# Performance work log

Measured on AMD Instinct MI355X. Metric: run time of the kernel, lower is better.

Reference implementation:

```python
import jax, jax.numpy as jnp
import numpy as np
from jax import lax

KS = 11          # kernel_size
SIGMA = 1.5
MAX_VAL = 1.0
K1, K2 = 0.01, 0.03


def _gauss2d(ks=KS, sigma=SIGMA):
    x = np.arange(ks, dtype=np.float64) - ks // 2
    g = np.exp(-(x ** 2) / (2.0 * sigma ** 2))
    g = g / g.sum()
    return np.outer(g, g).astype(np.float32)  # [ks, ks]


def _bilinear_matrix(n_in, n_out):
    # align_corners=True bilinear resize as a linear map [n_out, n_in]
    pos = np.arange(n_out, dtype=np.float64) * (n_in - 1) / (n_out - 1)
    i0 = np.floor(pos).astype(np.int64)
    i1 = np.minimum(i0 + 1, n_in - 1)
    w = (pos - i0).astype(np.float32)
    M = np.zeros((n_out, n_in), dtype=np.float32)
    M[np.arange(n_out), i0] += 1.0 - w
    M[np.arange(n_out), i1] += w
    return jnp.asarray(M)


def setup_inputs() -> dict:
    key = jax.random.key(0)
    k1, k2 = jax.random.split(key)
    inp = jax.random.uniform(k1, (32, 3, 384, 384), dtype=jnp.float32)
    tgt = jax.random.uniform(k2, (32, 3, 512, 512), dtype=jnp.float32)
    return {"input": inp, "target": tgt}


def _ssim_loss(input, target):
    B, C, Hi, Wi = input.shape
    Ho, Wo = target.shape[-2], target.shape[-1]
    # bilinear align_corners interpolation of input to target spatial size
    A = _bilinear_matrix(Hi, Ho)  # [Ho, Hi]
    Bm = _bilinear_matrix(Wi, Wo)  # [Wo, Wi]
    img1 = jnp.einsum('oh,bchw,pw->bcop', A, input, Bm)
    img2 = target

    w2d = jnp.asarray(_gauss2d())
    window = jnp.broadcast_to(w2d, (C, 1, KS, KS))  # depthwise kernel [C,1,k,k]

    def dwconv(x):
        return lax.conv_general_dilated(
            x, window, window_strides=(1, 1), padding='VALID',
            feature_group_count=C,
            dimension_numbers=('NCHW', 'OIHW', 'NCHW'))

    mu1 = dwconv(img1)
    mu2 = dwconv(img2)
    mu1_sq = mu1 * mu1
    mu2_sq = mu2 * mu2
    mu1_mu2 = mu1 * mu2
    sigma1_sq = dwconv(img1 * img1) - mu1_sq
    sigma2_sq = dwconv(img2 * img2) - mu2_sq
    sigma12 = dwconv(img1 * img2) - mu1_mu2

    C1 = (K1 * MAX_VAL) ** 2
    C2 = (K2 * MAX_VAL) ** 2
    v1 = 2.0 * sigma12 + C2
    v2 = sigma1_sq + sigma2_sq + C2
    ssim_map = (2.0 * mu1_mu2 + C1) * v1 / ((mu1_sq + mu2_sq + C1) * v2)
    ret = jnp.mean(ssim_map)
    return jnp.clip(1.0 - ret, 0.0, 1.0)


def reference(input, target):
    return _ssim_loss(input, target)
```

## Files before the change

### kernel.cpp

```cpp
#include <hip/hip_runtime.h>


constexpr int KS = 11;
constexpr int HI = 384, WI = 384, HO = 512, WO = 512;
constexpr int OUTD = 502;
constexpr int NPLANE = 96;
constexpr int CH_OUT = 32;
constexpr int NCHUNK = 16;
constexpr float C1 = 1.0e-4f;
constexpr float C2 = 9.0e-4f;

__device__ __constant__ float GW[KS] = {
    0.00102838f, 0.00759876f, 0.03600076f, 0.10936070f, 0.21300554f,
    0.26601172f, 0.21300554f, 0.10936070f, 0.03600076f, 0.00759876f, 0.00102838f};

__device__ __forceinline__ float ssim_term(float S, float D, float P, float M)
{
    float SS = S * S, DD = D * D;
    float mu12 = 0.25f * (SS - DD);
    float musq = 0.5f  * (SS + DD);
    float s12  = 0.25f * (P - M) - mu12;
    float ssum = 0.5f  * (P + M) - musq;
    float num = fmaf(2.f, mu12, C1) * fmaf(2.f, s12, C2);
    float den = (musq + C1) * (ssum + C2);
    return __fdividef(num, den);
}

__global__ __launch_bounds__(256, 3)
void ssim_stream(const float* __restrict__ input, const float* __restrict__ target,
                 double* __restrict__ accum)
{
    __shared__ float bs[2][WO];
    __shared__ float bd[2][WO];
    __shared__ float wave_sums[4];

    const int tid   = threadIdx.x;
    const int chunk = blockIdx.x;
    const int plane = blockIdx.y;
    const int oyb   = chunk * CH_OUT;
    const int nout  = min(CH_OUT, OUTD - oyb);
    const int rows  = nout + KS - 1;

    const int c0 = tid * 2, c1 = c0 + 1;

    int xA0, xA1, xB0, xB1; float wxA, wxB;
    {
        float pA = (float)(c0 * (WI - 1)) / (float)(WO - 1);
        xA0 = (int)pA; wxA = pA - (float)xA0; xA1 = min(xA0 + 1, WI - 1);
        float pB = (float)(c1 * (WI - 1)) / (float)(WO - 1);
        xB0 = (int)pB; wxB = pB - (float)xB0; xB1 = min(xB0 + 1, WI - 1);
    }

    const float* __restrict__ ip = input  + (size_t)plane * HI * WI;
    const float* __restrict__ tp = target + (size_t)plane * HO * WO;

    float aS[11][2], aD[11][2], aP[11][2], aM[11][2];
    #pragma unroll
    for (int s = 0; s < 11; ++s) {
        aS[s][0] = 0.f; aS[s][1] = 0.f; aD[s][0] = 0.f; aD[s][1] = 0.f;
        aP[s][0] = 0.f; aP[s][1] = 0.f; aM[s][0] = 0.f; aM[s][1] = 0.f;
    }

    float p00A, p01A, p10A, p11A, p00B, p01B, p10B, p11B, pt0, pt1, pwy;
    auto PRELOAD = [&](int r) {
        int y = oyb + r;
        float py = (float)(y * (HI - 1)) / (float)(HO - 1);
        int y0 = (int)py; pwy = py - (float)y0;
        int y1 = min(y0 + 1, HI - 1);
        const float* r0 = ip + y0 * WI;
        const float* r1 = ip + y1 * WI;
        p00A = r0[xA0]; p01A = r0[xA1]; p10A = r1[xA0]; p11A = r1[xA1];
        p00B = r0[xB0]; p01B = r0[xB1]; p10B = r1[xB0]; p11B = r1[xB1];
        float2 tv = *(const float2*)&tp[y * WO + c0];
        pt0 = tv.x; pt1 = tv.y;
    };

    float lsum = 0.f;
    PRELOAD(0);

    for (int t = 0; t < 4; ++t) {
        #pragma unroll
        for (int i = 0; i < 11; ++i) {
            const int r = t * 11 + i;
            if (r < rows) {
                const int p = r & 1;
                float topA = p00A + wxA * (p01A - p00A);
                float botA = p10A + wxA * (p11A - p10A);
                float a0 = topA + pwy * (botA - topA);
                float topB = p00B + wxB * (p01B - p00B);
                float botB = p10B + wxB * (p11B - p10B);
                float a1 = topB + pwy * (botB - topB);
                float s0 = a0 + pt0, d0 = a0 - pt0;
                float s1 = a1 + pt1, d1 = a1 - pt1;
                *(float2*)&bs[p][c0] = make_float2(s0, s1);
                *(float2*)&bd[p][c0] = make_float2(d0, d1);
                if (r + 1 < rows) PRELOAD(r + 1);
                __syncthreads();
                float sv[12], dv[12];
                #pragma unroll
                for (int j = 0; j < 6; ++j) {
                    float2 tS = *(const float2*)&bs[p][c0 + 2 * j];
                    float2 tD = *(const float2*)&bd[p][c0 + 2 * j];
                    sv[2 * j] = tS.x; sv[2 * j + 1] = tS.y;
                    dv[2 * j] = tD.x; dv[2 * j + 1] = tD.y;
                }
                float hS0 = 0.f, hS1 = 0.f, hD0 = 0.f, hD1 = 0.f;
                float hP0 = 0.f, hP1 = 0.f, hM0 = 0.f, hM1 = 0.f;
                float svp = sv[0], dvp = dv[0];
                float sqp = svp * svp, dqp = dvp * dvp;
                #pragma unroll
                for (int j = 0; j < 11; ++j) {
                    float svn = sv[j + 1], dvn = dv[j + 1];
                    float sqn = svn * svn, dqn = dvn * dvn;
                    float w = GW[j];
                    hS0 = fmaf(w, svp, hS0); hS1 = fmaf(w, svn, hS1);
                    hD0 = fmaf(w, dvp, hD0); hD1 = fmaf(w, dvn, hD1);
                    hP0 = fmaf(w, sqp, hP0); hP1 = fmaf(w, sqn, hP1);
                    hM0 = fmaf(w, dqp, hM0); hM1 = fmaf(w, dqn, hM1);
                    svp = svn; dvp = dvn; sqp = sqn; dqp = dqn;
                }
                #pragma unroll
                for (int j = 0; j < 11; ++j) {
                    const int sl = ((i - j) % 11 + 11) % 11;
                    float w = GW[j];
                    aS[sl][0] = fmaf(w, hS0, aS[sl][0]); aS[sl][1] = fmaf(w, hS1, aS[sl][1]);
                    aD[sl][0] = fmaf(w, hD0, aD[sl][0]); aD[sl][1] = fmaf(w, hD1, aD[sl][1]);
                    aP[sl][0] = fmaf(w, hP0, aP[sl][0]); aP[sl][1] = fmaf(w, hP1, aP[sl][1]);
                    aM[sl][0] = fmaf(w, hM0, aM[sl][0]); aM[sl][1] = fmaf(w, hM1, aM[sl][1]);
                }
                const int sf = (i + 1) % 11;
                if (r >= 10) {
                    if (c0 < OUTD) {
                        lsum += ssim_term(aS[sf][0], aD[sf][0], aP[sf][0], aM[sf][0]);
                        if (c1 < OUTD)
                            lsum += ssim_term(aS[sf][1], aD[sf][1], aP[sf][1], aM[sf][1]);
                    }
                }
                aS[sf][0] = 0.f; aS[sf][1] = 0.f; aD[sf][0] = 0.f; aD[sf][1] = 0.f;
                aP[sf][0] = 0.f; aP[sf][1] = 0.f; aM[sf][0] = 0.f; aM[sf][1] = 0.f;
            }
        }
    }

    #pragma unroll
    for (int off = 32; off > 0; off >>= 1) lsum += __shfl_down(lsum, off);
    int wave = tid >> 6, lane = tid & 63;
    if (lane == 0) wave_sums[wave] = lsum;
    __syncthreads();
    if (tid == 0) {
        float s = wave_sums[0] + wave_sums[1] + wave_sums[2] + wave_sums[3];
        atomicAdd(accum, (double)s);
    }
}

__global__ void ssim_finalize(const double* __restrict__ accum, float* __restrict__ out)
{
    if (threadIdx.x == 0 && blockIdx.x == 0) {
        double mean = accum[0] / ((double)NPLANE * OUTD * OUTD);
        double l = 1.0 - mean;
        if (l < 0.0) l = 0.0;
        if (l > 1.0) l = 1.0;
        out[0] = (float)l;
    }
}

extern "C" void kernel_launch(void* const* d_in, const int* in_sizes, int n_in,
                              void* d_out, int out_size, void* d_ws, size_t ws_size,
                              hipStream_t stream)
{
    const float* input  = (const float*)d_in[0];
    const float* target = (const float*)d_in[1];
    float* out = (float*)d_out;
    double* accum = (double*)d_ws;

    hipMemsetAsync(accum, 0, sizeof(double), stream);

    dim3 grid(NCHUNK, NPLANE);
    ssim_stream<<<grid, dim3(256), 0, stream>>>(input, target, accum);
    ssim_finalize<<<1, 64, 0, stream>>>(accum, out);
}
```

Before: 291.0 us.

## Pack S/D/squares into float4 LDS rows and double-buffer prefetch two rows ahead

Each thread now writes S, D, S² and D² into interleaved float4 shared arrays split into even and odd columns, so the horizontal pass does vectorised float4 loads and never recomputes squares from neighbours. Bilinear sampling shares three input taps between the two output columns, and the global prefetch now runs two rows ahead with a ping-pong register buffer. The row loop is unrolled into two blocks of 22 and launch bounds drop to 2 blocks per SM. The trade is more registers and larger LDS per block against fewer recomputed squares, wider LDS accesses and better latency hiding.

```diff
diff --git a/kernel.cpp b/kernel.cpp
--- a/kernel.cpp
+++ b/kernel.cpp
@@ -14,8 +14,16 @@
     0.00102838f, 0.00759876f, 0.03600076f, 0.10936070f, 0.21300554f,
     0.26601172f, 0.21300554f, 0.10936070f, 0.03600076f, 0.00759876f, 0.00102838f};
 
-__device__ __forceinline__ float ssim_term(float S, float D, float P, float M)
+__device__ __forceinline__ float4 f4fma(float w, float4 x, float4 a)
 {
+    a.x = fmaf(w, x.x, a.x); a.y = fmaf(w, x.y, a.y);
+    a.z = fmaf(w, x.z, a.z); a.w = fmaf(w, x.w, a.w);
+    return a;
+}
+
+__device__ __forceinline__ float ssim_term(float4 f)
+{
+    float S = f.x, D = f.y, P = f.z, M = f.w;
     float SS = S * S, DD = D * D;
     float mu12 = 0.25f * (SS - DD);
     float musq = 0.5f  * (SS + DD);
@@ -26,12 +34,12 @@
     return __fdividef(num, den);
 }
 
-__global__ __launch_bounds__(256, 3)
+__global__ __launch_bounds__(256, 2)
 void ssim_stream(const float* __restrict__ input, const float* __restrict__ target,
                  double* __restrict__ accum)
 {
-    __shared__ float bs[2][WO];
-    __shared__ float bd[2][WO];
+    __shared__ __align__(16) float4 chE[2][262];
+    __shared__ __align__(16) float4 chO[2][262];
     __shared__ float wave_sums[4];
 
     const int tid   = threadIdx.x;
@@ -41,103 +49,92 @@
     const int nout  = min(CH_OUT, OUTD - oyb);
     const int rows  = nout + KS - 1;
 
-    const int c0 = tid * 2, c1 = c0 + 1;
+    const int c0 = 2 * tid;
 
-    int xA0, xA1, xB0, xB1; float wxA, wxB;
-    {
-        float pA = (float)(c0 * (WI - 1)) / (float)(WO - 1);
-        xA0 = (int)pA; wxA = pA - (float)xA0; xA1 = min(xA0 + 1, WI - 1);
-        float pB = (float)(c1 * (WI - 1)) / (float)(WO - 1);
-        xB0 = (int)pB; wxB = pB - (float)xB0; xB1 = min(xB0 + 1, WI - 1);
-    }
+    float pA = (float)(c0 * (WI - 1)) / (float)(WO - 1);
+    int   xA0 = (int)pA; float wxA = pA - (float)xA0;
+    float pB = (float)((c0 + 1) * (WI - 1)) / (float)(WO - 1);
+    int   xB0 = (int)pB; float wxB = pB - (float)xB0;
+    const bool shift = (xB0 != xA0);
+    const int xs0 = xA0, xs1 = xA0 + 1, xs2 = min(xA0 + 2, WI - 1);
 
     const float* __restrict__ ip = input  + (size_t)plane * HI * WI;
     const float* __restrict__ tp = target + (size_t)plane * HO * WO;
 
-    float aS[11][2], aD[11][2], aP[11][2], aM[11][2];
+    float4 rA[11], rB[11];
     #pragma unroll
     for (int s = 0; s < 11; ++s) {
-        aS[s][0] = 0.f; aS[s][1] = 0.f; aD[s][0] = 0.f; aD[s][1] = 0.f;
-        aP[s][0] = 0.f; aP[s][1] = 0.f; aM[s][0] = 0.f; aM[s][1] = 0.f;
+        rA[s] = make_float4(0.f, 0.f, 0.f, 0.f);
+        rB[s] = make_float4(0.f, 0.f, 0.f, 0.f);
     }
 
-    float p00A, p01A, p10A, p11A, p00B, p01B, p10B, p11B, pt0, pt1, pwy;
-    auto PRELOAD = [&](int r) {
+    float u0[2], u1[2], u2[2], v0[2], v1[2], v2[2], wyp[2];
+    float2 tg[2];
+    auto PRELOAD = [&](int r, int sl) {
         int y = oyb + r;
         float py = (float)(y * (HI - 1)) / (float)(HO - 1);
-        int y0 = (int)py; pwy = py - (float)y0;
+        int y0 = (int)py; wyp[sl] = py - (float)y0;
         int y1 = min(y0 + 1, HI - 1);
         const float* r0 = ip + y0 * WI;
         const float* r1 = ip + y1 * WI;
-        p00A = r0[xA0]; p01A = r0[xA1]; p10A = r1[xA0]; p11A = r1[xA1];
-        p00B = r0[xB0]; p01B = r0[xB1]; p10B = r1[xB0]; p11B = r1[xB1];
-        float2 tv = *(const float2*)&tp[y * WO + c0];
-        pt0 = tv.x; pt1 = tv.y;
+        u0[sl] = r0[xs0]; u1[sl] = r0[xs1]; u2[sl] = r0[xs2];
+        v0[sl] = r1[xs0]; v1[sl] = r1[xs1]; v2[sl] = r1[xs2];
+        tg[sl] = *(const float2*)&tp[y * WO + c0];
     };
 
     float lsum = 0.f;
-    PRELOAD(0);
+    PRELOAD(0, 0);
+    PRELOAD(1, 1);
 
-    for (int t = 0; t < 4; ++t) {
+    for (int t = 0; t < 2; ++t) {
         #pragma unroll
-        for (int i = 0; i < 11; ++i) {
-            const int r = t * 11 + i;
+        for (int i = 0; i < 22; ++i) {
+            const int r = t * 22 + i;
             if (r < rows) {
-                const int p = r & 1;
-                float topA = p00A + wxA * (p01A - p00A);
-                float botA = p10A + wxA * (p11A - p10A);
-                float a0 = topA + pwy * (botA - topA);
-                float topB = p00B + wxB * (p01B - p00B);
-                float botB = p10B + wxB * (p11B - p10B);
-                float a1 = topB + pwy * (botB - topB);
-                float s0 = a0 + pt0, d0 = a0 - pt0;
-                float s1 = a1 + pt1, d1 = a1 - pt1;
-                *(float2*)&bs[p][c0] = make_float2(s0, s1);
-                *(float2*)&bd[p][c0] = make_float2(d0, d1);
-                if (r + 1 < rows) PRELOAD(r + 1);
+                const int p = i & 1;
+                float wy = wyp[p];
+                float V0 = fmaf(wy, v0[p] - u0[p], u0[p]);
+                float V1 = fmaf(wy, v1[p] - u1[p], u1[p]);
+                float V2 = fmaf(wy, v2[p] - u2[p], u2[p]);
+                float a0 = fmaf(wxA, V1 - V0, V0);
+                float bL = shift ? V1 : V0;
+                float bR = shift ? V2 : V1;
+                float a1 = fmaf(wxB, bR - bL, bL);
+                float2 tv = tg[p];
+                float s0 = a0 + tv.x, d0 = a0 - tv.x;
+                float s1 = a1 + tv.y, d1 = a1 - tv.y;
+                chE[p][tid] = make_float4(s0, d0, s0 * s0, d0 * d0);
+                chO[p][tid] = make_float4(s1, d1, s1 * s1, d1 * d1);
+                if (r + 2 < rows) PRELOAD(r + 2, p);
                 __syncthreads();
-                float sv[12], dv[12];
+                float4 acc0 = make_float4(0.f, 0.f, 0.f, 0.f);
+                float4 acc1 = make_float4(0.f, 0.f, 0.f, 0.f);
                 #pragma unroll
-                for (int j = 0; j < 6; ++j) {
-                    float2 tS = *(const float2*)&bs[p][c0 + 2 * j];
-                    float2 tD = *(const float2*)&bd[p][c0 + 2 * j];
-                    sv[2 * j] = tS.x; sv[2 * j + 1] = tS.y;
-                    dv[2 * j] = tD.x; dv[2 * j + 1] = tD.y;
+                for (int m = 0; m < 6; ++m) {
+                    float4 E = chE[p][tid + m];
+                    float4 O = chO[p][tid + m];
+                    float we = GW[2 * m];
+                    acc0 = f4fma(we, E, acc0);
+                    acc1 = f4fma(we, O, acc1);
+                    if (m < 5) acc0 = f4fma(GW[2 * m + 1], O, acc0);
+                    if (m >= 1) acc1 = f4fma(GW[2 * m - 1], E, acc1);
                 }
-                float hS0 = 0.f, hS1 = 0.f, hD0 = 0.f, hD1 = 0.f;
-                float hP0 = 0.f, hP1 = 0.f, hM0 = 0.f, hM1 = 0.f;
-                float svp = sv[0], dvp = dv[0];
-                float sqp = svp * svp, dqp = dvp * dvp;
+                const int im = i % 11;
                 #pragma unroll
                 for (int j = 0; j < 11; ++j) {
-                    float svn = sv[j + 1], dvn = dv[j + 1];
-                    float sqn = svn * svn, dqn = dvn * dvn;
-                    float w = GW[j];
-                    hS0 = fmaf(w, svp, hS0); hS1 = fmaf(w, svn, hS1);
-                    hD0 = fmaf(w, dvp, hD0); hD1 = fmaf(w, dvn, hD1);
-                    hP0 = fmaf(w, sqp, hP0); hP1 = fmaf(w, sqn, hP1);
-                    hM0 = fmaf(w, dqp, hM0); hM1 = fmaf(w, dqn, hM1);
-                    svp = svn; dvp = dvn; sqp = sqn; dqp = dqn;
+                    const int sl = (im - j + 11) % 11;
+                    rA[sl] = f4fma(GW[j], acc0, rA[sl]);
+                    rB[sl] = f4fma(GW[j], acc1, rB[sl]);
                 }
-                #pragma unroll
-                for (int j = 0; j < 11; ++j) {
-                    const int sl = ((i - j) % 11 + 11) % 11;
-                    float w = GW[j];
-                    aS[sl][0] = fmaf(w, hS0, aS[sl][0]); aS[sl][1] = fmaf(w, hS1, aS[sl][1]);
-                    aD[sl][0] = fmaf(w, hD0, aD[sl][0]); aD[sl][1] = fmaf(w, hD1, aD[sl][1]);
-                    aP[sl][0] = fmaf(w, hP0, aP[sl][0]); aP[sl][1] = fmaf(w, hP1, aP[sl][1]);
-                    aM[sl][0] = fmaf(w, hM0, aM[sl][0]); aM[sl][1] = fmaf(w, hM1, aM[sl][1]);
-                }
-                const int sf = (i + 1) % 11;
+                const int sf = (im + 1) % 11;
                 if (r >= 10) {
                     if (c0 < OUTD) {
-                        lsum += ssim_term(aS[sf][0], aD[sf][0], aP[sf][0], aM[sf][0]);
-                        if (c1 < OUTD)
-                            lsum += ssim_term(aS[sf][1], aD[sf][1], aP[sf][1], aM[sf][1]);
+                        lsum += ssim_term(rA[sf]);
+                        if (c0 + 1 < OUTD) lsum += ssim_term(rB[sf]);
                     }
                 }
-                aS[sf][0] = 0.f; aS[sf][1] = 0.f; aD[sf][0] = 0.f; aD[sf][1] = 0.f;
-                aP[sf][0] = 0.f; aP[sf][1] = 0.f; aM[sf][0] = 0.f; aM[sf][1] = 0.f;
+                rA[sf] = make_float4(0.f, 0.f, 0.f, 0.f);
+                rB[sf] = make_float4(0.f, 0.f, 0.f, 0.f);
             }
         }
     }
```

After: 309.1 us. +6.2%, slower.
